# Optimization experiments

Measured on AMD Instinct MI355X. Metric: run time of the kernel, lower is better.

The kernel has to match this reference:

```python
import jax, jax.numpy as jnp
import numpy as np

B, H1, W1 = 2, 64, 64
H2, W2 = 64, 64
DIM = 64    # query_latent_dim
CLD = 128   # cost_latent_dim
K = 8       # latent tokens in cost memory
HEADS = 8
CH = 1      # cost_heads_num
R = 4


def layer_norm(x, g, b, eps=1e-5):
    m = x.mean(-1, keepdims=True)
    v = ((x - m) ** 2).mean(-1, keepdims=True)
    return (x - m) / jnp.sqrt(v + eps) * g + b


def lin_pos_emb(x, dim):
    # LinearPositionEmbeddingSine: x [N,1,2] -> [N,1,dim]
    freq = jnp.linspace(0.0, dim // 4 - 1, dim // 4)
    a = 3.14 * x[..., 0:1] * freq / 200.0
    b = 3.14 * x[..., 1:2] * freq / 200.0
    return jnp.concatenate([jnp.sin(a), jnp.cos(a), jnp.sin(b), jnp.cos(b)], axis=-1)


def bilinear_sample(img, coords):
    # img: [N,C,H,W]; coords: [N,h,w,2] (x,y) pixel coords; zero padding, align_corners=True
    N, C, H, W = img.shape
    x, y = coords[..., 0], coords[..., 1]
    x0 = jnp.floor(x); y0 = jnp.floor(y)
    wx = x - x0; wy = y - y0
    nidx = jnp.arange(N)[:, None, None]

    def gather(xi, yi):
        valid = ((xi >= 0) & (xi <= W - 1) & (yi >= 0) & (yi <= H - 1)).astype(img.dtype)
        xc = jnp.clip(xi, 0, W - 1).astype(jnp.int32)
        yc = jnp.clip(yi, 0, H - 1).astype(jnp.int32)
        return img[nidx, :, yc, xc] * valid[..., None]  # [N,h,w,C]

    v00 = gather(x0, y0); v10 = gather(x0 + 1.0, y0)
    v01 = gather(x0, y0 + 1.0); v11 = gather(x0 + 1.0, y0 + 1.0)
    out = (v00 * ((1 - wx) * (1 - wy))[..., None] + v10 * (wx * (1 - wy))[..., None]
           + v01 * ((1 - wx) * wy)[..., None] + v11 * (wx * wy)[..., None])
    return out.transpose(0, 3, 1, 2)  # [N,C,h,w]


def encode_flow(cost_maps, coords1):
    b, _, h1, w1 = coords1.shape
    c = coords1.transpose(0, 2, 3, 1)  # [B,H1,W1,2]
    d = jnp.linspace(-float(R), float(R), 2 * R + 1)
    dy, dx = jnp.meshgrid(d, d, indexing='ij')
    delta = jnp.stack([dy, dx], axis=-1)  # [9,9,2]
    centroid = c.reshape(b * h1 * w1, 1, 1, 2)
    samp = centroid + delta[None]  # [B*H1*W1,9,9,2]
    corr = bilinear_sample(cost_maps, samp)  # [B*H1*W1,CH,9,9]
    return corr.reshape(b, h1, w1, -1).transpose(0, 3, 1, 2)  # [B,81*CH,H1,W1]


def upsample_flow(flow, mask):
    # convex upsample [H,W] -> [8H,8W]
    n, _, h, w = flow.shape
    m = jax.nn.softmax(mask.reshape(n, 1, 9, 8, 8, h, w), axis=2)
    f = jnp.pad(8.0 * flow, ((0, 0), (0, 0), (1, 1), (1, 1)))
    patches = jnp.stack([f[:, :, i:i + h, j:j + w] for i in range(3) for j in range(3)], axis=2)
    up = jnp.sum(m * patches[:, :, :, None, None], axis=2)  # [N,2,8,8,H,W]
    return up.transpose(0, 1, 4, 2, 5, 3).reshape(n, 2, 8 * h, 8 * w)


def setup_inputs() -> dict:
    key = jax.random.key(0)
    ks = jax.random.split(key, 16)
    Bn = B * H1 * W1
    ys, xs = np.meshgrid(np.arange(H1), np.arange(W1), indexing='ij')
    grid = jnp.asarray(np.stack([xs, ys], 0), jnp.float32)  # [2,H1,W1], (x,y)
    coords1 = jnp.broadcast_to(grid, (B, 2, H1, W1)) + 3.0 * jax.random.normal(ks[0], (B, 2, H1, W1), jnp.float32)
    s = 0.05
    return {
        'cost_maps': jax.random.normal(ks[1], (Bn, CH, H2, W2), jnp.float32),
        'cost_memory': jax.random.normal(ks[2], (Bn, K, CLD), jnp.float32),
        'coords1': coords1,
        'up_mask': jax.random.normal(ks[3], (B, 9 * 64, H1, W1), jnp.float32),
        'fte_w1': s * jax.random.normal(ks[4], (DIM, 81 * CH), jnp.float32),
        'fte_b1': jnp.zeros((DIM,), jnp.float32),
        'fte_w2': s * jax.random.normal(ks[5], (DIM, DIM), jnp.float32),
        'fte_b2': jnp.zeros((DIM,), jnp.float32),
        'ln1_g': jnp.ones((DIM,), jnp.float32),
        'ln1_b': jnp.zeros((DIM,), jnp.float32),
        'ln2_g': jnp.ones((DIM,), jnp.float32),
        'ln2_b': jnp.zeros((DIM,), jnp.float32),
        'wq': s * jax.random.normal(ks[6], (DIM, DIM), jnp.float32),
        'bq': jnp.zeros((DIM,), jnp.float32),
        'wk': s * jax.random.normal(ks[7], (CLD, DIM), jnp.float32),
        'bk': jnp.zeros((DIM,), jnp.float32),
        'wv': s * jax.random.normal(ks[8], (CLD, DIM), jnp.float32),
        'bv': jnp.zeros((DIM,), jnp.float32),
        'wp': s * jax.random.normal(ks[9], (2 * DIM, DIM), jnp.float32),
        'bp': jnp.zeros((DIM,), jnp.float32),
        'ffn_w1': s * jax.random.normal(ks[10], (DIM, DIM), jnp.float32),
        'ffn_b1': jnp.zeros((DIM,), jnp.float32),
        'ffn_w2': s * jax.random.normal(ks[11], (DIM, DIM), jnp.float32),
        'ffn_b2': jnp.zeros((DIM,), jnp.float32),
    }


def reference(cost_maps, cost_memory, coords1, up_mask,
              fte_w1, fte_b1, fte_w2, fte_b2,
              ln1_g, ln1_b, ln2_g, ln2_b,
              wq, bq, wk, bk, wv, bv, wp, bp,
              ffn_w1, ffn_b1, ffn_w2, ffn_b2):
    Bn = B * H1 * W1
    ys, xs = jnp.meshgrid(jnp.arange(H1, dtype=coords1.dtype), jnp.arange(W1, dtype=coords1.dtype), indexing='ij')
    coords0 = jnp.broadcast_to(jnp.stack([xs, ys], 0), (B, 2, H1, W1))

    # correlation-volume bilinear sampling (encode_flow_token)
    corr = encode_flow(cost_maps, coords1)  # [B,81*CH,H1,W1]

    # flow token encoder: 1x1 conv -> GELU -> 1x1 conv
    q = jnp.einsum('bchw,oc->bohw', corr, fte_w1) + fte_b1[None, :, None, None]
    q = jax.nn.gelu(q, approximate=False)
    q = jnp.einsum('bchw,oc->bohw', q, fte_w2) + fte_b2[None, :, None, None]
    query = q.transpose(0, 2, 3, 1).reshape(Bn, 1, DIM)

    # cross attention with linear sine position encoding of query coords
    qc = coords1.reshape(B, 2, H1 * W1).transpose(0, 2, 1).reshape(Bn, 1, 2)
    enc = lin_pos_emb(qc, DIM)
    short = query
    qn = layer_norm(query, ln1_g, ln1_b)
    qlin = (qn + enc) @ wq + bq            # [Bn,1,DIM]
    k = cost_memory @ wk + bk              # [Bn,K,DIM]
    v = cost_memory @ wv + bv
    hd = DIM // HEADS
    qh = qlin.reshape(Bn, 1, HEADS, hd).transpose(0, 2, 1, 3)
    kh = k.reshape(Bn, K, HEADS, hd).transpose(0, 2, 1, 3)
    vh = v.reshape(Bn, K, HEADS, hd).transpose(0, 2, 1, 3)
    attn = jax.nn.softmax(jnp.einsum('bhid,bhjd->bhij', qh, kh) * (hd ** -0.5), axis=-1)
    out = jnp.einsum('bhij,bhjd->bhid', attn, vh).transpose(0, 2, 1, 3).reshape(Bn, 1, DIM)
    x = jnp.concatenate([out, short], -1) @ wp + bp
    x = short + x
    xn = layer_norm(x, ln2_g, ln2_b)
    x = x + (jax.nn.gelu(xn @ ffn_w1 + ffn_b1, approximate=False) @ ffn_w2 + ffn_b2)
    cost_global = x.reshape(B, H1, W1, DIM).transpose(0, 3, 1, 2)

    # convex upsampling of the flow field
    flow_up = upsample_flow(coords1 - coords0, up_mask)  # [B,2,8*H1,8*W1]
    return (flow_up, cost_global)
```

## Files before the change

### kernel.cpp

```cpp
#include <hip/hip_runtime.h>
#include <math.h>

typedef _Float16 h2 __attribute__((ext_vector_type(2)));

#if __has_builtin(__builtin_amdgcn_fdot2)
#define FDOT2(a,b,c) __builtin_amdgcn_fdot2((a),(b),(c),false)
#else
__device__ __forceinline__ float FDOT2(h2 a, h2 b, float c){
    return c + (float)a.x*(float)b.x + (float)a.y*(float)b.y;
}
#endif

__device__ __forceinline__ h2 pk2(float x, float y){
#if __has_builtin(__builtin_amdgcn_cvt_pkrtz)
    return __builtin_bit_cast(h2, __builtin_amdgcn_cvt_pkrtz(x, y));
#else
    h2 r; r.x = (_Float16)x; r.y = (_Float16)y; return r;
#endif
}
__device__ __forceinline__ unsigned h2u(h2 v){ return __builtin_bit_cast(unsigned, v); }
__device__ __forceinline__ h2 uh2(unsigned v){ return __builtin_bit_cast(h2, v); }

__device__ __forceinline__ float fast_rcp(float x){
#if __has_builtin(__builtin_amdgcn_rcpf)
    return __builtin_amdgcn_rcpf(x);
#else
    return 1.f/x;
#endif
}

__device__ __forceinline__ float dot8(uint4 w, uint4 v, float acc){
    acc = FDOT2(uh2(w.x), uh2(v.x), acc);
    acc = FDOT2(uh2(w.y), uh2(v.y), acc);
    acc = FDOT2(uh2(w.z), uh2(v.z), acc);
    acc = FDOT2(uh2(w.w), uh2(v.w), acc);
    return acc;
}

__device__ __forceinline__ float gelu_exact(float x){
    return 0.5f * x * (1.0f + erff(x * 0.70710678118654752f));
}

__device__ __forceinline__ void ln_stats(float x, float& mean, float& inv){
    float s1 = x, s2 = x*x;
    #pragma unroll
    for(int off = 32; off >= 1; off >>= 1){
        s1 += __shfl_xor(s1, off, 64);
        s2 += __shfl_xor(s2, off, 64);
    }
    mean = s1 * (1.f/64.f);
    float var = fmaxf(s2 * (1.f/64.f) - mean*mean, 0.f);
    inv = rsqrtf(var + 1e-5f);
}

__device__ __forceinline__ void lds_fence(){ __asm__ volatile("s_waitcnt lgkmcnt(0)" ::: "memory"); }

#define W1T_OFF 0
#define W2T_OFF 2816
#define WQ_OFF  5120
#define FW1_OFF 7424
#define FW2_OFF 9728
#define WV_OFF  12032
#define WP_OFF  16384
#define WK_OFF  20736
#define WTOT    25344

#define CMO   0
#define TUO   544
#define CORRO 1088
#define QPO   1132
#define CCO   1168
#define PIXDW 1232
#define LDSDW (WTOT + 8*PIXDW)

__global__ void prep_weights(const float* __restrict__ w1, const float* __restrict__ w2,
                             const float* __restrict__ wq, const float* __restrict__ fw1,
                             const float* __restrict__ fw2, const float* __restrict__ wv,
                             const float* __restrict__ wp, const float* __restrict__ wk,
                             unsigned* __restrict__ ws){
    int idx = blockIdx.x * blockDim.x + threadIdx.x;
    if(idx >= WTOT) return;
    float a = 0.f, b = 0.f;
    if(idx < W2T_OFF){
        int t = idx / 44, cp = idx % 44;
        if(2*cp   < 81) a = w1[t*81 + 2*cp];
        if(2*cp+1 < 81) b = w1[t*81 + 2*cp+1];
    } else if(idx < WQ_OFF){
        int r = idx - W2T_OFF; int t = r / 36, cp = r % 36;
        if(cp < 32){ a = w2[t*64 + 2*cp]; b = w2[t*64 + 2*cp+1]; }
    } else if(idx < FW1_OFF){
        int r = idx - WQ_OFF; int t = r / 36, cp = r % 36;
        if(cp < 32){ a = wq[(2*cp)*64 + t]; b = wq[(2*cp+1)*64 + t]; }
    } else if(idx < FW2_OFF){
        int r = idx - FW1_OFF; int t = r / 36, cp = r % 36;
        if(cp < 32){ a = fw1[(2*cp)*64 + t]; b = fw1[(2*cp+1)*64 + t]; }
    } else if(idx < WV_OFF){
        int r = idx - FW2_OFF; int t = r / 36, cp = r % 36;
        if(cp < 32){ a = fw2[(2*cp)*64 + t]; b = fw2[(2*cp+1)*64 + t]; }
    } else if(idx < WP_OFF){
        int r = idx - WV_OFF; int t = r / 68, cp = r % 68;
        if(cp < 64){ a = wv[(2*cp)*64 + t]; b = wv[(2*cp+1)*64 + t]; }
    } else if(idx < WK_OFF){
        int r = idx - WK_OFF; int t = r / 68, cp = r % 68;
        if(cp < 64){ a = wp[(2*cp)*64 + t]; b = wp[(2*cp+1)*64 + t]; }
    } else {
        int r = idx - WK_OFF; int c = r / 36, hp = r % 36;
        if(hp < 32){ a = wk[c*64 + 2*hp]; b = wk[c*64 + 2*hp+1]; }
    }
    ws[idx] = h2u(pk2(a, b));
}

__device__ __forceinline__ float bilin(const float* __restrict__ cmap, float cx, float cy, int e){
    int i = e / 9, j = e - 9*i;
    float sx = cx + (float)(i - 4);
    float sy = cy + (float)(j - 4);
    float x0 = floorf(sx), y0 = floorf(sy);
    float wx = sx - x0,   wy = sy - y0;
    float acc = 0.f;
    #pragma unroll
    for(int dy = 0; dy < 2; dy++){
        #pragma unroll
        for(int dx = 0; dx < 2; dx++){
            float xf = x0 + (float)dx, yf = y0 + (float)dy;
            bool valid = (xf >= 0.f) && (xf <= 63.f) && (yf >= 0.f) && (yf <= 63.f);
            int xi = min(max((int)xf, 0), 63);
            int yi = min(max((int)yf, 0), 63);
            float v = valid ? cmap[yi*64 + xi] : 0.f;
            acc += v * ((dx ? wx : 1.f - wx) * (dy ? wy : 1.f - wy));
        }
    }
    return acc;
}

__global__ __launch_bounds__(512, 1) void decoder_main(
    const float* __restrict__ cost_maps, const float* __restrict__ cost_memory,
    const float* __restrict__ coords1, const float* __restrict__ up_mask,
    const unsigned* __restrict__ ws,
    const float* __restrict__ fte_b1, const float* __restrict__ fte_b2,
    const float* __restrict__ ln1_g, const float* __restrict__ ln1_b,
    const float* __restrict__ ln2_g, const float* __restrict__ ln2_b,
    const float* __restrict__ bq, const float* __restrict__ bv,
    const float* __restrict__ bp, const float* __restrict__ fb1,
    const float* __restrict__ fb2, float* __restrict__ out)
{
    __shared__ unsigned sm[LDSDW];

    const int tid = threadIdx.x;
    const int wv  = tid >> 6;
    const int ln  = tid & 63;

    int pix = blockIdx.x * 32 + wv;
    const float4* cm4p = (const float4*)cost_memory;
    float4 cmv0 = cm4p[(size_t)pix*256 +   0 + ln];
    float4 cmv1 = cm4p[(size_t)pix*256 +  64 + ln];
    float4 cmv2 = cm4p[(size_t)pix*256 + 128 + ln];
    float4 cmv3 = cm4p[(size_t)pix*256 + 192 + ln];
    float cx = coords1[(pix >> 12)*8192 + (pix & 4095)];
    float cy = coords1[(pix >> 12)*8192 + 4096 + (pix & 4095)];

    {
        const uint4* src = (const uint4*)ws;
        uint4* dst = (uint4*)sm;
        for(int i = tid; i < WTOT/4; i += 512) dst[i] = src[i];
    }
    const float b1v = fte_b1[ln], b2v = fte_b2[ln];
    const float g1v = ln1_g[ln], be1 = ln1_b[ln];
    const float g2v = ln2_g[ln], be2 = ln2_b[ln];
    const float bqv = bq[ln], bvv = bv[ln], bpv = bp[ln];
    const float f1v = fb1[ln], f2v = fb2[ln];
    __syncthreads();

    float* out_cg = out + 2*2*512*512;
    unsigned* P = sm + WTOT + wv * PIXDW;

    const int h_ = ln & 7;
    const int c0 = ln >> 3;
    const int j_ = ln >> 3;
    const int h3 = ln >> 3;

    #pragma unroll 1
    for(int g = 0; g < 4; g++){
        {
            float4 v; int l0, jt, cp0;
            #define STAGE(V, I4) \
                v = V; l0 = 4*((I4)*64 + ln); jt = l0 >> 7; cp0 = (l0 & 127) >> 1; \
                { uint2 pw; pw.x = h2u(pk2(v.x, v.y)); pw.y = h2u(pk2(v.z, v.w)); \
                  *(uint2*)&P[CMO + jt*68 + cp0] = pw; }
            STAGE(cmv0, 0) STAGE(cmv1, 1) STAGE(cmv2, 2) STAGE(cmv3, 3)
            #undef STAGE
        }
        {
            const float* cmap = cost_maps + (size_t)pix * 4096;
            float cv = bilin(cmap, cx, cy, ln);
            float c2 = bilin(cmap, cx, cy, 64 + ln);
            float pr = __shfl_xor(cv, 1, 64);
            if((ln & 1) == 0) P[CORRO + (ln >> 1)] = h2u(pk2(cv, pr));
            float pr2 = __shfl_xor(c2, 1, 64);
            if(ln < 17 && (ln & 1) == 0){
                float bb = (ln == 16) ? 0.f : pr2;
                P[CORRO + 32 + (ln >> 1)] = h2u(pk2(c2, bb));
            }
            if(ln < 3) P[CORRO + 41 + ln] = 0u;
        }
        int npix = pix + 8;
        float4 n0, n1, n2, n3; float ncx = 0.f, ncy = 0.f;
        if(g < 3){
            n0 = cm4p[(size_t)npix*256 +   0 + ln];
            n1 = cm4p[(size_t)npix*256 +  64 + ln];
            n2 = cm4p[(size_t)npix*256 + 128 + ln];
            n3 = cm4p[(size_t)npix*256 + 192 + ln];
            ncx = coords1[(npix >> 12)*8192 + (npix & 4095)];
            ncy = coords1[(npix >> 12)*8192 + 4096 + (npix & 4095)];
        }
        lds_fence();

        float q1;
        {
            const uint4* wr = (const uint4*)&sm[W1T_OFF + ln*44];
            const uint4* ar = (const uint4*)&P[CORRO];
            float a0 = b1v, a1 = 0.f;
            #pragma unroll
            for(int gg = 0; gg < 10; gg += 2){
                a0 = dot8(wr[gg],   ar[gg],   a0);
                a1 = dot8(wr[gg+1], ar[gg+1], a1);
            }
            a0 = dot8(wr[10], ar[10], a0);
            q1 = a0 + a1;
        }
        q1 = gelu_exact(q1);
        {
            float pr = __shfl_xor(q1, 1, 64);
            if((ln & 1) == 0) P[QPO + (ln >> 1)] = h2u(pk2(q1, pr));
        }
        lds_fence();
        float shortv;
        {
            const uint4* wr = (const uint4*)&sm[W2T_OFF + ln*36];
            const uint4* ar = (const uint4*)&P[QPO];
            float a0 = b2v, a1 = 0.f;
            #pragma unroll
            for(int gg = 0; gg < 8; gg += 2){
                a0 = dot8(wr[gg],   ar[gg],   a0);
                a1 = dot8(wr[gg+1], ar[gg+1], a1);
            }
            shortv = a0 + a1;
        }
        {
            float psv = __shfl_xor(shortv, 1, 64);
            if((ln & 1) == 0) P[CCO + 32 + (ln >> 1)] = h2u(pk2(shortv, psv));
        }
        float mean, inv1;
        ln_stats(shortv, mean, inv1);
        float qn = (shortv - mean) * inv1 * g1v + be1;
        {
            int   fi    = ln & 15;
            float coord = (ln < 32) ? cx : cy;
            float ang   = 3.14f * coord * (float)fi / 200.0f;
            float enc   = (ln & 16) ? __cosf(ang) : __sinf(ang);
            float qv    = qn + enc;
            float pr = __shfl_xor(qv, 1, 64);
            if((ln & 1) == 0) P[QPO + (ln >> 1)] = h2u(pk2(qv, pr));
        }
        lds_fence();
        float qlin;
        {
            const uint4* wr = (const uint4*)&sm[WQ_OFF + ln*36];
            const uint4* ar = (const uint4*)&P[QPO];
            float a0 = bqv, a1 = 0.f;
            #pragma unroll
            for(int gg = 0; gg < 8; gg += 2){
                a0 = dot8(wr[gg],   ar[gg],   a0);
                a1 = dot8(wr[gg+1], ar[gg+1], a1);
            }
            qlin = a0 + a1;
        }
        {
            float pr = __shfl_xor(qlin, 1, 64);
            if((ln & 1) == 0) P[QPO + (ln >> 1)] = h2u(pk2(qlin, pr));
        }
        lds_fence();
        {
            uint4 qh4 = *(const uint4*)&P[QPO + h_*4];
            #pragma unroll
            for(int i = 0; i < 16; i++){
                int c = c0 + 8*i;
                uint4 wk4 = *(const uint4*)&sm[WK_OFF + c*36 + h_*4];
                float tv = dot8(wk4, qh4, 0.f);
                float prt = __shfl_xor(tv, 8, 64);
                if((c0 & 1) == 0) P[TUO + h_*68 + (c0 >> 1) + 4*i] = h2u(pk2(tv, prt));
            }
        }
        lds_fence();
        float sacc;
        {
            const int hk = ln & 7;
            const uint4* cmr = (const uint4*)&P[CMO + j_*68];
            const uint4* tur = (const uint4*)&P[TUO + hk*68];
            float s0 = 0.f, s1 = 0.f, s2 = 0.f, s3 = 0.f;
            #pragma unroll
            for(int gg = 0; gg < 16; gg += 4){
                s0 = dot8(cmr[gg],   tur[gg],   s0);
                s1 = dot8(cmr[gg+1], tur[gg+1], s1);
                s2 = dot8(cmr[gg+2], tur[gg+2], s2);
                s3 = dot8(cmr[gg+3], tur[gg+3], s3);
            }
            sacc = (s0 + s1) + (s2 + s3);
        }
        float p;
        {
            float sc = sacc * 0.35355339059327373f;
            float mx = sc;
            mx = fmaxf(mx, __shfl_xor(mx,  8, 64));
            mx = fmaxf(mx, __shfl_xor(mx, 16, 64));
            mx = fmaxf(mx, __shfl_xor(mx, 32, 64));
            float ex = __expf(sc - mx);
            float se = ex;
            se += __shfl_xor(se,  8, 64);
            se += __shfl_xor(se, 16, 64);
            se += __shfl_xor(se, 32, 64);
            p = ex * fast_rcp(se);
        }
        {
            float av[8];
            #pragma unroll
            for(int j = 0; j < 8; j++) av[j] = __shfl(p, j*8 + h_, 64);
            h2 u0 = pk2(0.f,0.f), u1 = u0, u2 = u0, u3 = u0;
            h2 u4 = u0, u5 = u0, u6 = u0, u7 = u0;
            #pragma unroll
            for(int j = 0; j < 8; j++){
                h2 aj = pk2(av[j], av[j]);
                const uint4* cmr = (const uint4*)&P[CMO + j*68 + 8*c0];
                uint4 qa = cmr[0], qb = cmr[1];
                u0 += aj * uh2(qa.x); u1 += aj * uh2(qa.y);
                u2 += aj * uh2(qa.z); u3 += aj * uh2(qa.w);
                u4 += aj * uh2(qb.x); u5 += aj * uh2(qb.y);
                u6 += aj * uh2(qb.z); u7 += aj * uh2(qb.w);
            }
            uint4 wa; wa.x = h2u(u0); wa.y = h2u(u1); wa.z = h2u(u2); wa.w = h2u(u3);
            uint4 wb; wb.x = h2u(u4); wb.y = h2u(u5); wb.z = h2u(u6); wb.w = h2u(u7);
            *(uint4*)&P[TUO + h_*68 + 8*c0]     = wa;
            *(uint4*)&P[TUO + h_*68 + 8*c0 + 4] = wb;
        }
        lds_fence();
        float attno;
        {
            const uint4* ur = (const uint4*)&P[TUO + h3*68];
            const uint4* wr = (const uint4*)&sm[WV_OFF + ln*68];
            float a0 = bvv, a1 = 0.f, a2 = 0.f, a3 = 0.f;
            #pragma unroll
            for(int gg = 0; gg < 16; gg += 4){
                a0 = dot8(ur[gg],   wr[gg],   a0);
                a1 = dot8(ur[gg+1], wr[gg+1], a1);
                a2 = dot8(ur[gg+2], wr[gg+2], a2);
                a3 = dot8(ur[gg+3], wr[gg+3], a3);
            }
            attno = (a0 + a1) + (a2 + a3);
        }
        {
            float pa = __shfl_xor(attno, 1, 64);
            if((ln & 1) == 0) P[CCO + (ln >> 1)] = h2u(pk2(attno, pa));
        }
        lds_fence();
        float x;
        {
            const uint4* wr = (const uint4*)&sm[WP_OFF + ln*68];
            const uint4* ar = (const uint4*)&P[CCO];
            float a0 = bpv, a1 = 0.f, a2 = 0.f, a3 = 0.f;
            #pragma unroll
            for(int gg = 0; gg < 16; gg += 4){
                a0 = dot8(wr[gg],   ar[gg],   a0);
                a1 = dot8(wr[gg+1], ar[gg+1], a1);
                a2 = dot8(wr[gg+2], ar[gg+2], a2);
                a3 = dot8(wr[gg+3], ar[gg+3], a3);
            }
            x = (a0 + a1) + (a2 + a3);
        }
        x += shortv;
        float m2, inv2;
        ln_stats(x, m2, inv2);
        float xn = (x - m2) * inv2 * g2v + be2;
        {
            float pr = __shfl_xor(xn, 1, 64);
            if((ln & 1) == 0) P[QPO + (ln >> 1)] = h2u(pk2(xn, pr));
        }
        lds_fence();
        float h1v;
        {
            const uint4* wr = (const uint4*)&sm[FW1_OFF + ln*36];
            const uint4* ar = (const uint4*)&P[QPO];
            float a0 = f1v, a1 = 0.f;
            #pragma unroll
            for(int gg = 0; gg < 8; gg += 2){
                a0 = dot8(wr[gg],   ar[gg],   a0);
                a1 = dot8(wr[gg+1], ar[gg+1], a1);
            }
            h1v = a0 + a1;
        }
        h1v = gelu_exact(h1v);
        {
            float pr = __shfl_xor(h1v, 1, 64);
            if((ln & 1) == 0) P[QPO + (ln >> 1)] = h2u(pk2(h1v, pr));
        }
        lds_fence();
        float f2;
        {
            const uint4* wr = (const uint4*)&sm[FW2_OFF + ln*36];
            const uint4* ar = (const uint4*)&P[QPO];
            float a0 = f2v, a1 = 0.f;
            #pragma unroll
            for(int gg = 0; gg < 8; gg += 2){
                a0 = dot8(wr[gg],   ar[gg],   a0);
                a1 = dot8(wr[gg+1], ar[gg+1], a1);
            }
            f2 = a0 + a1;
        }
        x += f2;
        {
            int bb = pix >> 12, hh = (pix >> 6) & 63, ww = pix & 63;
            out_cg[(((size_t)(bb*64 + ln))*64 + hh)*64 + ww] = x;
        }
        pix = npix; cx = ncx; cy = ncy;
        cmv0 = n0; cmv1 = n1; cmv2 = n2; cmv3 = n3;
    }

    {
        const int U  = blockIdx.x * 4 + (wv >> 1);
        const int sh = (wv & 1) * 4;
        const int ub = U >> 9, uh = (U >> 3) & 63, ur = U & 7;
        const int w  = ln;

        float fx[3], fy[3];
        #pragma unroll
        for(int i = 0; i < 3; i++){
            int hh = uh + i - 1;
            bool ok = (hh >= 0) && (hh < 64);
            int hc = min(max(hh, 0), 63);
            float cxv = coords1[((ub*2 + 0)*64 + hc)*64 + w];
            float cyv = coords1[((ub*2 + 1)*64 + hc)*64 + w];
            fx[i] = ok ? 8.f * (cxv - (float)w)  : 0.f;
            fy[i] = ok ? 8.f * (cyv - (float)hh) : 0.f;
        }
        float fxm[3], fxp[3], fym[3], fyp[3];
        #pragma unroll
        for(int i = 0; i < 3; i++){
            fxm[i] = __shfl(fx[i], w - 1, 64);
            fxp[i] = __shfl(fx[i], w + 1, 64);
            fym[i] = __shfl(fy[i], w - 1, 64);
            fyp[i] = __shfl(fy[i], w + 1, 64);
            if(w == 0) { fxm[i] = 0.f; fym[i] = 0.f; }
            if(w == 63){ fxp[i] = 0.f; fyp[i] = 0.f; }
        }
        float m[36];
        #pragma unroll
        for(int k = 0; k < 9; k++){
            #pragma unroll
            for(int si = 0; si < 4; si++){
                int c = k*64 + ur*8 + sh + si;
                m[k*4 + si] = up_mask[(((size_t)ub*576 + c)*64 + uh)*64 + w];
            }
        }
        float outx[4], outy[4];
        #pragma unroll
        for(int si = 0; si < 4; si++){
            float mx = m[si];
            #pragma unroll
            for(int k = 1; k < 9; k++) mx = fmaxf(mx, m[k*4 + si]);
            float e, se = 0.f, ox = 0.f, oy = 0.f;
            #pragma unroll
            for(int k = 0; k < 9; k++){
                e = __expf(m[k*4 + si] - mx);
                se += e;
                int i = k / 3, j = k % 3;
                float fxv = (j == 0) ? fxm[i] : ((j == 1) ? fx[i] : fxp[i]);
                float fyv = (j == 0) ? fym[i] : ((j == 1) ? fy[i] : fyp[i]);
                ox += e * fxv;
                oy += e * fyv;
            }
            float inv = fast_rcp(se);
            outx[si] = ox * inv;
            outy[si] = oy * inv;
        }
        size_t row = (size_t)(uh*8 + ur) * 512 + w*8 + sh;
        *(float4*)&out[(size_t)(ub*2 + 0)*262144 + row] = *(const float4*)outx;
        *(float4*)&out[(size_t)(ub*2 + 1)*262144 + row] = *(const float4*)outy;
    }
}

extern "C" void kernel_launch(void* const* d_in, const int* in_sizes, int n_in,
                              void* d_out, int out_size, void* d_ws, size_t ws_size,
                              hipStream_t stream)
{
    const float* cost_maps   = (const float*)d_in[0];
    const float* cost_memory = (const float*)d_in[1];
    const float* coords1     = (const float*)d_in[2];
    const float* up_mask     = (const float*)d_in[3];
    const float* fte_w1      = (const float*)d_in[4];
    const float* fte_b1      = (const float*)d_in[5];
    const float* fte_w2      = (const float*)d_in[6];
    const float* fte_b2      = (const float*)d_in[7];
    const float* ln1_g       = (const float*)d_in[8];
    const float* ln1_b       = (const float*)d_in[9];
    const float* ln2_g       = (const float*)d_in[10];
    const float* ln2_b       = (const float*)d_in[11];
    const float* wq          = (const float*)d_in[12];
    const float* bq          = (const float*)d_in[13];
    const float* wk          = (const float*)d_in[14];
    const float* bv          = (const float*)d_in[17];
    const float* wv          = (const float*)d_in[16];
    const float* wp          = (const float*)d_in[18];
    const float* bp          = (const float*)d_in[19];
    const float* fw1         = (const float*)d_in[20];
    const float* fb1         = (const float*)d_in[21];
    const float* fw2         = (const float*)d_in[22];
    const float* fb2         = (const float*)d_in[23];
    float* out = (float*)d_out;
    unsigned* wsu = (unsigned*)d_ws;

    prep_weights<<<(WTOT + 511)/512, 512, 0, stream>>>(
        fte_w1, fte_w2, wq, fw1, fw2, wv, wp, wk, wsu);

    decoder_main<<<256, 512, 0, stream>>>(
        cost_maps, cost_memory, coords1, up_mask, wsu,
        fte_b1, fte_b2, ln1_g, ln1_b, ln2_g, ln2_b,
        bq, bv, bp, fb1, fb2,
        out);
}
```

Before: 265.6 us.

## Rebalance decoder work across 12 waves per block with strided pixel assignment

Each block now runs 768 threads (12 waves) instead of 512, and the 8192 pixels are spread across 3072 global waves in a stride of 3072, so each wave handles 2 or 3 pixels. The upsample work goes only to the waves that get two pixels, and each of those does a full row of 8 subpixels in two halves, which balances load across waves. The per-pixel LDS scratch is shrunk by overlaying the correlation buffer on the TU region, and the query-head exchange now uses cross-lane shuffles instead of an LDS round trip. It also corrects the wp offset in prep_weights, which changes numerics, and the larger block raises register pressure per thread.

```diff
diff --git a/kernel.cpp b/kernel.cpp
--- a/kernel.cpp
+++ b/kernel.cpp
@@ -67,11 +67,12 @@
 
 #define CMO   0
 #define TUO   544
-#define CORRO 1088
-#define QPO   1132
-#define CCO   1168
-#define PIXDW 1232
-#define LDSDW (WTOT + 8*PIXDW)
+#define CORRO 544
+#define QPO   1088
+#define CCO   1124
+#define PIXDW 1188
+#define NWAVES 12
+#define LDSDW (WTOT + NWAVES*PIXDW)
 
 __global__ void prep_weights(const float* __restrict__ w1, const float* __restrict__ w2,
                              const float* __restrict__ wq, const float* __restrict__ fw1,
@@ -101,7 +102,7 @@
         int r = idx - WV_OFF; int t = r / 68, cp = r % 68;
         if(cp < 64){ a = wv[(2*cp)*64 + t]; b = wv[(2*cp+1)*64 + t]; }
     } else if(idx < WK_OFF){
-        int r = idx - WK_OFF; int t = r / 68, cp = r % 68;
+        int r = idx - WP_OFF; int t = r / 68, cp = r % 68;
         if(cp < 64){ a = wp[(2*cp)*64 + t]; b = wp[(2*cp+1)*64 + t]; }
     } else {
         int r = idx - WK_OFF; int c = r / 36, hp = r % 36;
@@ -132,7 +133,7 @@
     return acc;
 }
 
-__global__ __launch_bounds__(512, 1) void decoder_main(
+__global__ __launch_bounds__(768, 1) void decoder_main(
     const float* __restrict__ cost_maps, const float* __restrict__ cost_memory,
     const float* __restrict__ coords1, const float* __restrict__ up_mask,
     const unsigned* __restrict__ ws,
@@ -148,8 +149,10 @@
     const int tid = threadIdx.x;
     const int wv  = tid >> 6;
     const int ln  = tid & 63;
-
-    int pix = blockIdx.x * 32 + wv;
+    const int gw  = blockIdx.x * NWAVES + wv;
+    const int nPix = (gw < 2048) ? 3 : 2;
+
+    int pix = gw;
     const float4* cm4p = (const float4*)cost_memory;
     float4 cmv0 = cm4p[(size_t)pix*256 +   0 + ln];
     float4 cmv1 = cm4p[(size_t)pix*256 +  64 + ln];
@@ -161,7 +164,7 @@
     {
         const uint4* src = (const uint4*)ws;
         uint4* dst = (uint4*)sm;
-        for(int i = tid; i < WTOT/4; i += 512) dst[i] = src[i];
+        for(int i = tid; i < WTOT/4; i += 768) dst[i] = src[i];
     }
     const float b1v = fte_b1[ln], b2v = fte_b2[ln];
     const float g1v = ln1_g[ln], be1 = ln1_b[ln];
@@ -179,7 +182,7 @@
     const int h3 = ln >> 3;
 
     #pragma unroll 1
-    for(int g = 0; g < 4; g++){
+    for(int g = 0; g < nPix; g++){
         {
             float4 v; int l0, jt, cp0;
             #define STAGE(V, I4) \
@@ -202,9 +205,9 @@
             }
             if(ln < 3) P[CORRO + 41 + ln] = 0u;
         }
-        int npix = pix + 8;
+        int npix = pix + 3072;
         float4 n0, n1, n2, n3; float ncx = 0.f, ncy = 0.f;
-        if(g < 3){
+        if(g + 1 < nPix){
             n0 = cm4p[(size_t)npix*256 +   0 + ln];
             n1 = cm4p[(size_t)npix*256 +  64 + ln];
             n2 = cm4p[(size_t)npix*256 + 128 + ln];
@@ -275,12 +278,15 @@
             qlin = a0 + a1;
         }
         {
-            float pr = __shfl_xor(qlin, 1, 64);
-            if((ln & 1) == 0) P[QPO + (ln >> 1)] = h2u(pk2(qlin, pr));
-        }
-        lds_fence();
-        {
-            uint4 qh4 = *(const uint4*)&P[QPO + h_*4];
+            uint4 qh4;
+            {
+                float v0 = __shfl(qlin, h_*8 + 0, 64), v1 = __shfl(qlin, h_*8 + 1, 64);
+                float v2 = __shfl(qlin, h_*8 + 2, 64), v3 = __shfl(qlin, h_*8 + 3, 64);
+                float v4 = __shfl(qlin, h_*8 + 4, 64), v5 = __shfl(qlin, h_*8 + 5, 64);
+                float v6 = __shfl(qlin, h_*8 + 6, 64), v7 = __shfl(qlin, h_*8 + 7, 64);
+                qh4.x = h2u(pk2(v0, v1)); qh4.y = h2u(pk2(v2, v3));
+                qh4.z = h2u(pk2(v4, v5)); qh4.w = h2u(pk2(v6, v7));
+            }
             #pragma unroll
             for(int i = 0; i < 16; i++){
                 int c = c0 + 8*i;
@@ -423,10 +429,9 @@
         cmv0 = n0; cmv1 = n1; cmv2 = n2; cmv3 = n3;
     }
 
-    {
-        const int U  = blockIdx.x * 4 + (wv >> 1);
-        const int sh = (wv & 1) * 4;
-        const int ub = U >> 9, uh = (U >> 3) & 63, ur = U & 7;
+    if(gw >= 2048){
+        const int u  = gw - 2048;
+        const int ub = u >> 9, uh = (u >> 3) & 63, ur = u & 7;
         const int w  = ln;
 
         float fx[3], fy[3];
@@ -450,39 +455,42 @@
             if(w == 0) { fxm[i] = 0.f; fym[i] = 0.f; }
             if(w == 63){ fxp[i] = 0.f; fyp[i] = 0.f; }
         }
-        float m[36];
         #pragma unroll
-        for(int k = 0; k < 9; k++){
+        for(int sh = 0; sh < 8; sh += 4){
+            float m[36];
+            #pragma unroll
+            for(int k = 0; k < 9; k++){
+                #pragma unroll
+                for(int si = 0; si < 4; si++){
+                    int c = k*64 + ur*8 + sh + si;
+                    m[k*4 + si] = up_mask[(((size_t)ub*576 + c)*64 + uh)*64 + w];
+                }
+            }
+            float outx[4], outy[4];
             #pragma unroll
             for(int si = 0; si < 4; si++){
-                int c = k*64 + ur*8 + sh + si;
-                m[k*4 + si] = up_mask[(((size_t)ub*576 + c)*64 + uh)*64 + w];
-            }
-        }
-        float outx[4], outy[4];
-        #pragma unroll
-        for(int si = 0; si < 4; si++){
-            float mx = m[si];
-            #pragma unroll
-            for(int k = 1; k < 9; k++) mx = fmaxf(mx, m[k*4 + si]);
-            float e, se = 0.f, ox = 0.f, oy = 0.f;
-            #pragma unroll
-            for(int k = 0; k < 9; k++){
-                e = __expf(m[k*4 + si] - mx);
-                se += e;
-                int i = k / 3, j = k % 3;
-                float fxv = (j == 0) ? fxm[i] : ((j == 1) ? fx[i] : fxp[i]);
-                float fyv = (j == 0) ? fym[i] : ((j == 1) ? fy[i] : fyp[i]);
-                ox += e * fxv;
-                oy += e * fyv;
-            }
-            float inv = fast_rcp(se);
-            outx[si] = ox * inv;
-            outy[si] = oy * inv;
-        }
-        size_t row = (size_t)(uh*8 + ur) * 512 + w*8 + sh;
-        *(float4*)&out[(size_t)(ub*2 + 0)*262144 + row] = *(const float4*)outx;
-        *(float4*)&out[(size_t)(ub*2 + 1)*262144 + row] = *(const float4*)outy;
+                float mx = m[si];
+                #pragma unroll
+                for(int k = 1; k < 9; k++) mx = fmaxf(mx, m[k*4 + si]);
+                float e, se = 0.f, ox = 0.f, oy = 0.f;
+                #pragma unroll
+                for(int k = 0; k < 9; k++){
+                    e = __expf(m[k*4 + si] - mx);
+                    se += e;
+                    int i = k / 3, j = k % 3;
+                    float fxv = (j == 0) ? fxm[i] : ((j == 1) ? fx[i] : fxp[i]);
+                    float fyv = (j == 0) ? fym[i] : ((j == 1) ? fy[i] : fyp[i]);
+                    ox += e * fxv;
+                    oy += e * fyv;
+                }
+                float inv = fast_rcp(se);
+                outx[si] = ox * inv;
+                outy[si] = oy * inv;
+            }
+            size_t row = (size_t)(uh*8 + ur) * 512 + w*8 + sh;
+            *(float4*)&out[(size_t)(ub*2 + 0)*262144 + row] = *(const float4*)outx;
+            *(float4*)&out[(size_t)(ub*2 + 1)*262144 + row] = *(const float4*)outy;
+        }
     }
 }
 
@@ -519,7 +527,7 @@
     prep_weights<<<(WTOT + 511)/512, 512, 0, stream>>>(
         fte_w1, fte_w2, wq, fw1, fw2, wv, wp, wk, wsu);
 
-    decoder_main<<<256, 512, 0, stream>>>(
+    decoder_main<<<256, 768, 0, stream>>>(
         cost_maps, cost_memory, coords1, up_mask, wsu,
         fte_b1, fte_b2, ln1_g, ln1_b, ln2_g, ln2_b,
         bq, bv, bp, fb1, fb2,
```

Measured after the change: 259.0 us. 2.5% less time.
